# Performance work log

Hardware: AMD Instinct MI355X
Metric: run time of the kernel (lower is better)

## Reference

```python
import jax, jax.numpy as jnp
import numpy as np

# Llama-3-8B-like attention, prefill over B sequences of length S (flattened tokens)
D = 4096      # hidden_size
N = 32        # num query heads
K = 8         # num KV heads (GQA)
H = 128       # head_dim (== head_dim_original, already a multiple of 128 so no padding)
B = 4         # sequences in the ragged batch
S = 1024      # tokens per sequence
T = B * S     # total flattened tokens
ROPE_THETA = 10000.0


def _apply_rope(x, positions, head_dim, theta):
    # x: [T, n_heads, H]; positions: [T] int
    inv_freq = 1.0 / (theta ** (jnp.arange(0, head_dim, 2, dtype=jnp.float32) / head_dim))
    freqs = positions.astype(jnp.float32)[:, None] * inv_freq[None, :]  # [T, H/2]
    emb = jnp.concatenate([freqs, freqs], axis=-1)                       # [T, H]
    cos = jnp.cos(emb)[:, None, :].astype(x.dtype)
    sin = jnp.sin(emb)[:, None, :].astype(x.dtype)
    x1, x2 = jnp.split(x, 2, axis=-1)
    rotated = jnp.concatenate([-x2, x1], axis=-1)
    return x * cos + rotated * sin


def setup_inputs() -> dict:
    key = jax.random.key(0)
    ks = jax.random.split(key, 5)
    x = jax.random.normal(ks[0], (T, D), dtype=jnp.float32)
    # positions restart per sequence (ragged prefill metadata)
    input_positions = (jnp.arange(T, dtype=jnp.int32) % S)
    w_scale = 0.02
    Wq = jax.random.normal(ks[1], (D, N, H), dtype=jnp.float32) * w_scale
    Wk = jax.random.normal(ks[2], (D, K, H), dtype=jnp.float32) * w_scale
    Wv = jax.random.normal(ks[3], (D, K, H), dtype=jnp.float32) * w_scale
    Wo = jax.random.normal(ks[4], (N, H, D), dtype=jnp.float32) * w_scale
    return {"x": x, "input_positions": input_positions,
            "Wq": Wq, "Wk": Wk, "Wv": Wv, "Wo": Wo}


def reference(x, input_positions, Wq, Wk, Wv, Wo):
    # QKV projections (flattened tokens)
    q = jnp.einsum('td,dnh->tnh', x, Wq)   # [T, N, H]
    k = jnp.einsum('td,dkh->tkh', x, Wk)   # [T, K, H]
    v = jnp.einsum('td,dkh->tkh', x, Wv)   # [T, K, H]
    q = _apply_rope(q, input_positions, H, ROPE_THETA)
    k = _apply_rope(k, input_positions, H, ROPE_THETA)

    # Ragged causal attention: per-sequence causal SDPA with GQA head grouping.
    G = N // K  # query heads per KV head
    qb = q.reshape(B, S, K, G, H)
    kb = k.reshape(B, S, K, H)
    vb = v.reshape(B, S, K, H)
    scale = jnp.asarray(H, q.dtype) ** -0.5  # head_dim_original ** -0.5
    scores = jnp.einsum('bqkgh,bskh->bkgqs', qb, kb) * scale  # [B,K,G,S,S]
    causal = jnp.tril(jnp.ones((S, S), dtype=bool))
    scores = jnp.where(causal, scores, jnp.finfo(scores.dtype).min)
    probs = jax.nn.softmax(scores, axis=-1)
    out = jnp.einsum('bkgqs,bskh->bqkgh', probs, vb).reshape(T, N, H)

    # Output projection
    o = jnp.einsum('tnh,nhd->td', out, Wo)  # [T, D]
    return o
```

## Files before the change

### kernel.cpp

```cpp
#include <hip/hip_runtime.h>
#include <cstdint>


typedef unsigned short u16;
typedef short bf16x8 __attribute__((ext_vector_type(8)));
typedef float f32x4 __attribute__((ext_vector_type(4)));

#define L2E 1.44269504088896340736f

static __device__ __forceinline__ u16 f2bf(float f) {
  union { float f; unsigned u; } v; v.f = f;
  unsigned r = (v.u + 0x7fffu + ((v.u >> 16) & 1u)) >> 16;
  return (u16)r;
}
static __device__ __forceinline__ float bf2f(u16 h) {
  union { unsigned u; float f; } v; v.u = ((unsigned)h) << 16;
  return v.f;
}

typedef __attribute__((address_space(1))) const unsigned int gas_u32;
typedef __attribute__((address_space(3))) unsigned int las_u32;
static __device__ __forceinline__ void glds16(const void* g, const void* l) {
  __builtin_amdgcn_global_load_lds((gas_u32*)(uintptr_t)g,
                                   (las_u32*)(unsigned)(uintptr_t)l, 16, 0, 0);
}

__global__ __launch_bounds__(256) void cvt_kernel(const float4* __restrict__ in,
                                                  uint2* __restrict__ out, int n4) {
  int i = blockIdx.x * 256 + threadIdx.x;
  if (i < n4) {
    float4 v = in[i];
    uint2 r;
    r.x = (unsigned)f2bf(v.x) | ((unsigned)f2bf(v.y) << 16);
    r.y = (unsigned)f2bf(v.z) | ((unsigned)f2bf(v.w) << 16);
    out[i] = r;
  }
}

__global__ __launch_bounds__(256) void tcvt_kernel(const float* __restrict__ in,
                                                   u16* __restrict__ out, int R, int C) {
  __shared__ float tile[32][33];
  int tx = threadIdx.x, ty = threadIdx.y;
  int r0 = blockIdx.y * 32, c0 = blockIdx.x * 32;
#pragma unroll
  for (int j = 0; j < 4; ++j)
    tile[ty + j * 8][tx] = in[(size_t)(r0 + ty + j * 8) * C + c0 + tx];
  __syncthreads();
#pragma unroll
  for (int j = 0; j < 4; ++j)
    out[(size_t)(c0 + ty + j * 8) * R + r0 + tx] = f2bf(tile[tx][ty + j * 8]);
}

template <int BF16OUT>
__global__ __launch_bounds__(256, 2) void gemm_nt(const u16* __restrict__ A,
                                                  const u16* __restrict__ Bm,
                                                  void* __restrict__ Cp,
                                                  int M, int N, int Kd) {
  __shared__ u16 Al[128 * 64];
  __shared__ u16 Bl[128 * 64];
  const int tid = threadIdx.x;
  const int w = tid >> 6, lane = tid & 63;
  const int ln15 = lane & 15, quad = lane >> 4;
  const int wm = w & 1, wn = w >> 1;
  const int m0 = blockIdx.y * 128, n0 = blockIdx.x * 128;

  const int rA = w * 8 + (lane >> 3);
  const int cA = (((lane & 7) ^ (rA & 7)) << 3);
  const u16* aptr = A + (size_t)(m0 + rA) * Kd + cA;
  const u16* bptr = Bm + (size_t)(n0 + rA) * Kd + cA;

  f32x4 acc[4][4];
#pragma unroll
  for (int i = 0; i < 4; ++i)
#pragma unroll
    for (int j = 0; j < 4; ++j) acc[i][j] = f32x4{0.f, 0.f, 0.f, 0.f};

  for (int k0 = 0; k0 < Kd; k0 += 64) {
    __syncthreads();
#pragma unroll
    for (int q = 0; q < 4; ++q) {
      glds16(aptr + (size_t)q * 32 * Kd, &Al[(q * 32 + w * 8) * 64]);
      glds16(bptr + (size_t)q * 32 * Kd, &Bl[(q * 32 + w * 8) * 64]);
    }
    aptr += 64; bptr += 64;
    __syncthreads();
#pragma unroll
    for (int ks = 0; ks < 2; ++ks) {
      bf16x8 af[4], bfr[4];
#pragma unroll
      for (int t = 0; t < 4; ++t) {
        int ra = wm * 64 + t * 16 + ln15;
        int pa = (ks * 4 + quad) ^ (ra & 7);
        af[t] = *(const bf16x8*)&Al[ra * 64 + pa * 8];
        int rb = wn * 64 + t * 16 + ln15;
        int pb = (ks * 4 + quad) ^ (rb & 7);
        bfr[t] = *(const bf16x8*)&Bl[rb * 64 + pb * 8];
      }
#pragma unroll
      for (int mt = 0; mt < 4; ++mt)
#pragma unroll
        for (int nt = 0; nt < 4; ++nt)
          acc[mt][nt] =
              __builtin_amdgcn_mfma_f32_16x16x32_bf16(af[mt], bfr[nt], acc[mt][nt], 0, 0, 0);
    }
  }

#pragma unroll
  for (int mt = 0; mt < 4; ++mt) {
#pragma unroll
    for (int nt = 0; nt < 4; ++nt) {
      int row = m0 + wm * 64 + mt * 16 + quad * 4;
      int col = n0 + wn * 64 + nt * 16 + ln15;
#pragma unroll
      for (int r = 0; r < 4; ++r) {
        float v = acc[mt][nt][r];
        if (BF16OUT)
          ((u16*)Cp)[(size_t)(row + r) * N + col] = f2bf(v);
        else
          ((float*)Cp)[(size_t)(row + r) * N + col] = v;
      }
    }
  }
}

__global__ __launch_bounds__(256) void rope_kernel(u16* __restrict__ qkv,
                                                   const int* __restrict__ pos) {
  int idx = blockIdx.x * 256 + threadIdx.x;
  int t = idx >> 6;
  int i = idx & 63;
  float p = (float)pos[t];
  float inv = exp2f(-0.20751874963942190927f * (float)i);
  float s, c;
  sincosf(p * inv, &s, &c);
  u16* base = qkv + (size_t)t * 6144 + i;
  const float qs = 0.08838834764831845f;
#pragma unroll 8
  for (int head = 0; head < 40; ++head) {
    int colbase = (head < 32) ? head * 128 : (4096 + (head - 32) * 128);
    u16* bp = base + colbase;
    float x1 = bf2f(bp[0]), x2 = bf2f(bp[64]);
    float o1 = x1 * c - x2 * s;
    float o2 = x2 * c + x1 * s;
    if (head < 32) { o1 *= qs; o2 *= qs; }
    bp[0] = f2bf(o1);
    bp[64] = f2bf(o2);
  }
}

__global__ __launch_bounds__(256, 2) void attn_kernel(const u16* __restrict__ qkv,
                                                      u16* __restrict__ outp) {
  __shared__ u16 Klds[64 * 128];
  __shared__ u16 Vtlds[128 * 72];
  __shared__ u16 Plds[4 * 32 * 72];

  const int bx = blockIdx.x;
  const int qb = 7 - (bx & 7);
  const int n = (bx >> 3) & 31;
  const int b = bx >> 8;
  const int kh = n >> 2;

  const int tid = threadIdx.x;
  const int w = tid >> 6;
  const int lane = tid & 63;
  const int ln15 = lane & 15;
  const int quad = lane >> 4;

  const int ldq = 6144;
  const int seq0 = b << 10;
  const int ql0 = qb * 128 + w * 32;
  const int q0g = seq0 + qb * 128;

  const u16* Qg = qkv + n * 128;
  const u16* Kg = qkv + 4096 + kh * 128;
  const u16* Vg = qkv + 5120 + kh * 128;

  bf16x8 qf[2][4];
#pragma unroll
  for (int mt = 0; mt < 2; ++mt) {
    const u16* qrow = Qg + (size_t)(q0g + w * 32 + mt * 16 + ln15) * ldq + quad * 8;
#pragma unroll
    for (int ks = 0; ks < 4; ++ks) qf[mt][ks] = *(const bf16x8*)(qrow + ks * 32);
  }

  f32x4 o[2][8];
#pragma unroll
  for (int mt = 0; mt < 2; ++mt)
#pragma unroll
    for (int i = 0; i < 8; ++i) o[mt][i] = f32x4{0.f, 0.f, 0.f, 0.f};
  float m_r[2][4], l_r[2][4];
#pragma unroll
  for (int mt = 0; mt < 2; ++mt)
#pragma unroll
    for (int r = 0; r < 4; ++r) { m_r[mt][r] = -INFINITY; l_r[mt][r] = 0.f; }

  const int krow = w * 4 + (lane >> 4);
  const int kcol = (((lane & 15) ^ (krow & 7)) << 3);

  const int vh0 = w * 32;

  const int ktiles = 2 * qb + 2;
  for (int kt = 0; kt < ktiles; ++kt) {
    __syncthreads();
    {
      const u16* kbase = Kg + (size_t)(seq0 + kt * 64 + krow) * ldq + kcol;
#pragma unroll
      for (int q = 0; q < 4; ++q)
        glds16(kbase + (size_t)q * 16 * ldq, &Klds[(q * 16 + w * 4) * 128]);
    }
    {
      const u16* v0 = Vg + (size_t)(seq0 + kt * 64 + lane) * ldq + vh0;
      union { uint4 v[4]; u16 s[32]; } rr;
      rr.v[0] = *(const uint4*)v0;
      rr.v[1] = *(const uint4*)(v0 + 8);
      rr.v[2] = *(const uint4*)(v0 + 16);
      rr.v[3] = *(const uint4*)(v0 + 24);
#pragma unroll
      for (int j = 0; j < 32; ++j)
        Vtlds[(vh0 + j) * 72 + lane] = rr.s[j];
    }
    __syncthreads();

    if (kt * 64 > ql0 + 31) continue;

#pragma unroll
    for (int mt = 0; mt < 2; ++mt) {
      f32x4 sfr[4];
#pragma unroll
      for (int c = 0; c < 4; ++c) {
        f32x4 acc = f32x4{0.f, 0.f, 0.f, 0.f};
#pragma unroll
        for (int ks = 0; ks < 4; ++ks) {
          int rk = c * 16 + ln15;
          int ph = (ks * 4 + quad) ^ (rk & 7);
          bf16x8 kf = *(const bf16x8*)&Klds[rk * 128 + ph * 8];
          acc = __builtin_amdgcn_mfma_f32_16x16x32_bf16(qf[mt][ks], kf, acc, 0, 0, 0);
        }
        sfr[c] = acc;
      }

      if (kt * 64 + 63 > ql0 + mt * 16) {
#pragma unroll
        for (int c = 0; c < 4; ++c) {
          int col = kt * 64 + c * 16 + ln15;
#pragma unroll
          for (int r = 0; r < 4; ++r)
            if (col > ql0 + mt * 16 + quad * 4 + r) sfr[c][r] = -INFINITY;
        }
      }

#pragma unroll
      for (int r = 0; r < 4; ++r) {
        float mx = fmaxf(fmaxf(sfr[0][r], sfr[1][r]), fmaxf(sfr[2][r], sfr[3][r]));
        mx = fmaxf(mx, __shfl_xor(mx, 1));
        mx = fmaxf(mx, __shfl_xor(mx, 2));
        mx = fmaxf(mx, __shfl_xor(mx, 4));
        mx = fmaxf(mx, __shfl_xor(mx, 8));
        float mnew = fmaxf(m_r[mt][r], mx);
        float al = exp2f((m_r[mt][r] - mnew) * L2E);
        m_r[mt][r] = mnew;
        float rs = 0.f;
#pragma unroll
        for (int c = 0; c < 4; ++c) {
          float pv = exp2f((sfr[c][r] - mnew) * L2E);
          sfr[c][r] = pv;
          rs += pv;
        }
        rs += __shfl_xor(rs, 1);
        rs += __shfl_xor(rs, 2);
        rs += __shfl_xor(rs, 4);
        rs += __shfl_xor(rs, 8);
        l_r[mt][r] = al * l_r[mt][r] + rs;
#pragma unroll
        for (int ht = 0; ht < 8; ++ht) o[mt][ht][r] *= al;
      }

#pragma unroll
      for (int c = 0; c < 4; ++c)
#pragma unroll
        for (int r = 0; r < 4; ++r)
          Plds[w * 2304 + (mt * 16 + quad * 4 + r) * 72 + c * 16 + ln15] =
              f2bf(sfr[c][r]);
    }

    asm volatile("s_waitcnt lgkmcnt(0)" ::: "memory");

#pragma unroll
    for (int mt = 0; mt < 2; ++mt) {
      bf16x8 pf[2];
#pragma unroll
      for (int ks = 0; ks < 2; ++ks)
        pf[ks] = *(const bf16x8*)&Plds[w * 2304 + (mt * 16 + ln15) * 72 + ks * 32 + quad * 8];
#pragma unroll
      for (int ht = 0; ht < 8; ++ht) {
#pragma unroll
        for (int ks = 0; ks < 2; ++ks) {
          bf16x8 vf = *(const bf16x8*)&Vtlds[(ht * 16 + ln15) * 72 + ks * 32 + quad * 8];
          o[mt][ht] = __builtin_amdgcn_mfma_f32_16x16x32_bf16(pf[ks], vf, o[mt][ht], 0, 0, 0);
        }
      }
    }
  }

#pragma unroll
  for (int mt = 0; mt < 2; ++mt)
#pragma unroll
    for (int r = 0; r < 4; ++r) l_r[mt][r] = 1.f / l_r[mt][r];
#pragma unroll
  for (int mt = 0; mt < 2; ++mt)
#pragma unroll
    for (int ht = 0; ht < 8; ++ht)
#pragma unroll
      for (int r = 0; r < 4; ++r)
        outp[(size_t)(q0g + w * 32 + mt * 16 + quad * 4 + r) * 4096 + n * 128 + ht * 16 + ln15] =
            f2bf(o[mt][ht][r] * l_r[mt][r]);
}

extern "C" void kernel_launch(void* const* d_in, const int* in_sizes, int n_in,
                              void* d_out, int out_size, void* d_ws, size_t ws_size,
                              hipStream_t stream) {
  const float* x = (const float*)d_in[0];
  const int* posi = (const int*)d_in[1];
  const float* Wq = (const float*)d_in[2];
  const float* Wk = (const float*)d_in[3];
  const float* Wv = (const float*)d_in[4];
  const float* Wo = (const float*)d_in[5];
  float* out = (float*)d_out;
  char* ws = (char*)d_ws;

  u16* xb = (u16*)(ws);
  u16* Wt = (u16*)(ws + 33554432);
  u16* WoT = (u16*)(ws + 83886080);
  u16* qkv = (u16*)(ws + 117440512);
  u16* attn = xb;

  cvt_kernel<<<16384, 256, 0, stream>>>((const float4*)x, (uint2*)xb, 4194304);
  tcvt_kernel<<<dim3(128, 128), dim3(32, 8), 0, stream>>>(Wq, Wt, 4096, 4096);
  tcvt_kernel<<<dim3(32, 128), dim3(32, 8), 0, stream>>>(Wk, Wt + (size_t)4096 * 4096, 4096, 1024);
  tcvt_kernel<<<dim3(32, 128), dim3(32, 8), 0, stream>>>(Wv, Wt + (size_t)5120 * 4096, 4096, 1024);
  tcvt_kernel<<<dim3(128, 128), dim3(32, 8), 0, stream>>>(Wo, WoT, 4096, 4096);

  gemm_nt<1><<<dim3(48, 32), 256, 0, stream>>>(xb, Wt, qkv, 4096, 6144, 4096);
  rope_kernel<<<1024, 256, 0, stream>>>(qkv, posi);
  attn_kernel<<<1024, 256, 0, stream>>>(qkv, attn);
  gemm_nt<0><<<dim3(32, 32), 256, 0, stream>>>(attn, WoT, out, 4096, 4096, 4096);
}
```

Measured before the change: 786.6 us.

## Split QKV output into separate Q, K and pre-transposed V buffers for attention

The QKV GEMM epilogue now writes Q, K and a transposed V into separate compact buffers instead of one interleaved 6144-wide array. The attention kernel then loads V tiles with direct global-to-LDS copies into a swizzled layout, replacing the per-thread register transpose and scalar LDS stores. Occupancy is also raised via launch bounds (3 blocks per SM). The cost is strided 8-byte scattered writes for V^T in the GEMM epilogue and higher register pressure risk from the new launch bound.

```diff
diff --git a/kernel.cpp b/kernel.cpp
--- a/kernel.cpp
+++ b/kernel.cpp
@@ -51,10 +51,12 @@
     out[(size_t)(c0 + ty + j * 8) * R + r0 + tx] = f2bf(tile[tx][ty + j * 8]);
 }
 
-template <int BF16OUT>
+template <int MODE>
 __global__ __launch_bounds__(256, 2) void gemm_nt(const u16* __restrict__ A,
                                                   const u16* __restrict__ Bm,
                                                   void* __restrict__ Cp,
+                                                  u16* __restrict__ kb,
+                                                  u16* __restrict__ vT,
                                                   int M, int N, int Kd) {
   __shared__ u16 Al[128 * 64];
   __shared__ u16 Bl[128 * 64];
@@ -111,19 +113,32 @@
     for (int nt = 0; nt < 4; ++nt) {
       int row = m0 + wm * 64 + mt * 16 + quad * 4;
       int col = n0 + wn * 64 + nt * 16 + ln15;
-#pragma unroll
-      for (int r = 0; r < 4; ++r) {
-        float v = acc[mt][nt][r];
-        if (BF16OUT)
-          ((u16*)Cp)[(size_t)(row + r) * N + col] = f2bf(v);
-        else
-          ((float*)Cp)[(size_t)(row + r) * N + col] = v;
-      }
-    }
-  }
-}
-
-__global__ __launch_bounds__(256) void rope_kernel(u16* __restrict__ qkv,
+      if (MODE == 0) {
+#pragma unroll
+        for (int r = 0; r < 4; ++r)
+          ((float*)Cp)[(size_t)(row + r) * N + col] = acc[mt][nt][r];
+      } else {
+        if (col < 4096) {
+#pragma unroll
+          for (int r = 0; r < 4; ++r)
+            ((u16*)Cp)[(size_t)(row + r) * 4096 + col] = f2bf(acc[mt][nt][r]);
+        } else if (col < 5120) {
+#pragma unroll
+          for (int r = 0; r < 4; ++r)
+            kb[(size_t)(row + r) * 1024 + (col - 4096)] = f2bf(acc[mt][nt][r]);
+        } else {
+          uint2 pk;
+          pk.x = (unsigned)f2bf(acc[mt][nt][0]) | ((unsigned)f2bf(acc[mt][nt][1]) << 16);
+          pk.y = (unsigned)f2bf(acc[mt][nt][2]) | ((unsigned)f2bf(acc[mt][nt][3]) << 16);
+          *(uint2*)&vT[(size_t)(col - 5120) * 4096 + row] = pk;
+        }
+      }
+    }
+  }
+}
+
+__global__ __launch_bounds__(256) void rope_kernel(u16* __restrict__ qb,
+                                                   u16* __restrict__ kb,
                                                    const int* __restrict__ pos) {
   int idx = blockIdx.x * 256 + threadIdx.x;
   int t = idx >> 6;
@@ -132,29 +147,35 @@
   float inv = exp2f(-0.20751874963942190927f * (float)i);
   float s, c;
   sincosf(p * inv, &s, &c);
-  u16* base = qkv + (size_t)t * 6144 + i;
   const float qs = 0.08838834764831845f;
+  u16* qp = qb + (size_t)t * 4096 + i;
 #pragma unroll 8
-  for (int head = 0; head < 40; ++head) {
-    int colbase = (head < 32) ? head * 128 : (4096 + (head - 32) * 128);
-    u16* bp = base + colbase;
+  for (int h = 0; h < 32; ++h) {
+    u16* bp = qp + h * 128;
     float x1 = bf2f(bp[0]), x2 = bf2f(bp[64]);
-    float o1 = x1 * c - x2 * s;
-    float o2 = x2 * c + x1 * s;
-    if (head < 32) { o1 *= qs; o2 *= qs; }
-    bp[0] = f2bf(o1);
-    bp[64] = f2bf(o2);
-  }
-}
-
-__global__ __launch_bounds__(256, 2) void attn_kernel(const u16* __restrict__ qkv,
+    bp[0] = f2bf((x1 * c - x2 * s) * qs);
+    bp[64] = f2bf((x2 * c + x1 * s) * qs);
+  }
+  u16* kp = kb + (size_t)t * 1024 + i;
+#pragma unroll
+  for (int h = 0; h < 8; ++h) {
+    u16* bp = kp + h * 128;
+    float x1 = bf2f(bp[0]), x2 = bf2f(bp[64]);
+    bp[0] = f2bf(x1 * c - x2 * s);
+    bp[64] = f2bf(x2 * c + x1 * s);
+  }
+}
+
+__global__ __launch_bounds__(256, 3) void attn_kernel(const u16* __restrict__ qb,
+                                                      const u16* __restrict__ kb,
+                                                      const u16* __restrict__ vT,
                                                       u16* __restrict__ outp) {
   __shared__ u16 Klds[64 * 128];
-  __shared__ u16 Vtlds[128 * 72];
+  __shared__ u16 Vt[128 * 64];
   __shared__ u16 Plds[4 * 32 * 72];
 
   const int bx = blockIdx.x;
-  const int qb = 7 - (bx & 7);
+  const int qb_i = 7 - (bx & 7);
   const int n = (bx >> 3) & 31;
   const int b = bx >> 8;
   const int kh = n >> 2;
@@ -165,19 +186,18 @@
   const int ln15 = lane & 15;
   const int quad = lane >> 4;
 
-  const int ldq = 6144;
   const int seq0 = b << 10;
-  const int ql0 = qb * 128 + w * 32;
-  const int q0g = seq0 + qb * 128;
-
-  const u16* Qg = qkv + n * 128;
-  const u16* Kg = qkv + 4096 + kh * 128;
-  const u16* Vg = qkv + 5120 + kh * 128;
+  const int ql0 = qb_i * 128 + w * 32;
+  const int q0g = seq0 + qb_i * 128;
+
+  const u16* Qg = qb + n * 128;
+  const u16* Kg = kb + kh * 128;
+  const u16* Vg = vT + (size_t)(kh * 128) * 4096;
 
   bf16x8 qf[2][4];
 #pragma unroll
   for (int mt = 0; mt < 2; ++mt) {
-    const u16* qrow = Qg + (size_t)(q0g + w * 32 + mt * 16 + ln15) * ldq + quad * 8;
+    const u16* qrow = Qg + (size_t)(q0g + w * 32 + mt * 16 + ln15) * 4096 + quad * 8;
 #pragma unroll
     for (int ks = 0; ks < 4; ++ks) qf[mt][ks] = *(const bf16x8*)(qrow + ks * 32);
   }
@@ -195,28 +215,23 @@
 
   const int krow = w * 4 + (lane >> 4);
   const int kcol = (((lane & 15) ^ (krow & 7)) << 3);
-
-  const int vh0 = w * 32;
-
-  const int ktiles = 2 * qb + 2;
+  const int vrA = w * 8 + (lane >> 3);
+  const int vcA = (((lane & 7) ^ (vrA & 7)) << 3);
+
+  const int ktiles = 2 * qb_i + 2;
   for (int kt = 0; kt < ktiles; ++kt) {
     __syncthreads();
     {
-      const u16* kbase = Kg + (size_t)(seq0 + kt * 64 + krow) * ldq + kcol;
+      const u16* kbase = Kg + (size_t)(seq0 + kt * 64 + krow) * 1024 + kcol;
 #pragma unroll
       for (int q = 0; q < 4; ++q)
-        glds16(kbase + (size_t)q * 16 * ldq, &Klds[(q * 16 + w * 4) * 128]);
+        glds16(kbase + (size_t)q * 16 * 1024, &Klds[(q * 16 + w * 4) * 128]);
     }
     {
-      const u16* v0 = Vg + (size_t)(seq0 + kt * 64 + lane) * ldq + vh0;
-      union { uint4 v[4]; u16 s[32]; } rr;
-      rr.v[0] = *(const uint4*)v0;
-      rr.v[1] = *(const uint4*)(v0 + 8);
-      rr.v[2] = *(const uint4*)(v0 + 16);
-      rr.v[3] = *(const uint4*)(v0 + 24);
-#pragma unroll
-      for (int j = 0; j < 32; ++j)
-        Vtlds[(vh0 + j) * 72 + lane] = rr.s[j];
+      const u16* vbase = Vg + (size_t)vrA * 4096 + (seq0 + kt * 64) + vcA;
+#pragma unroll
+      for (int q = 0; q < 4; ++q)
+        glds16(vbase + (size_t)q * 32 * 4096, &Vt[(q * 32 + w * 8) * 64]);
     }
     __syncthreads();
 
@@ -294,7 +309,9 @@
       for (int ht = 0; ht < 8; ++ht) {
 #pragma unroll
         for (int ks = 0; ks < 2; ++ks) {
-          bf16x8 vf = *(const bf16x8*)&Vtlds[(ht * 16 + ln15) * 72 + ks * 32 + quad * 8];
+          int hrow = ht * 16 + ln15;
+          int ph = (ks * 4 + quad) ^ (hrow & 7);
+          bf16x8 vf = *(const bf16x8*)&Vt[hrow * 64 + ph * 8];
           o[mt][ht] = __builtin_amdgcn_mfma_f32_16x16x32_bf16(pf[ks], vf, o[mt][ht], 0, 0, 0);
         }
       }
@@ -327,10 +344,12 @@
   float* out = (float*)d_out;
   char* ws = (char*)d_ws;
 
-  u16* xb = (u16*)(ws);
-  u16* Wt = (u16*)(ws + 33554432);
-  u16* WoT = (u16*)(ws + 83886080);
-  u16* qkv = (u16*)(ws + 117440512);
+  u16* xb   = (u16*)(ws);
+  u16* Wt   = (u16*)(ws + 33554432);
+  u16* WoT  = (u16*)(ws + 83886080);
+  u16* qbuf = (u16*)(ws + 117440512);
+  u16* kbuf = (u16*)(ws + 150994944);
+  u16* vTb  = (u16*)(ws + 159383552);
   u16* attn = xb;
 
   cvt_kernel<<<16384, 256, 0, stream>>>((const float4*)x, (uint2*)xb, 4194304);
@@ -339,8 +358,8 @@
   tcvt_kernel<<<dim3(32, 128), dim3(32, 8), 0, stream>>>(Wv, Wt + (size_t)5120 * 4096, 4096, 1024);
   tcvt_kernel<<<dim3(128, 128), dim3(32, 8), 0, stream>>>(Wo, WoT, 4096, 4096);
 
-  gemm_nt<1><<<dim3(48, 32), 256, 0, stream>>>(xb, Wt, qkv, 4096, 6144, 4096);
-  rope_kernel<<<1024, 256, 0, stream>>>(qkv, posi);
-  attn_kernel<<<1024, 256, 0, stream>>>(qkv, attn);
-  gemm_nt<0><<<dim3(32, 32), 256, 0, stream>>>(attn, WoT, out, 4096, 4096, 4096);
-}
+  gemm_nt<1><<<dim3(48, 32), 256, 0, stream>>>(xb, Wt, qbuf, kbuf, vTb, 4096, 6144, 4096);
+  rope_kernel<<<1024, 256, 0, stream>>>(qbuf, kbuf, posi);
+  attn_kernel<<<1024, 256, 0, stream>>>(qbuf, kbuf, vTb, attn);
+  gemm_nt<0><<<dim3(32, 32), 256, 0, stream>>>(attn, WoT, out, nullptr, nullptr, 4096, 4096, 4096);
+}
```

Result: slower. 875.7 us (+11.3%).
